# Performance work log

Hardware: AMD Instinct MI355X
Metric: run time of the kernel (lower is better)

The kernel has to match this reference:

```python
import jax, jax.numpy as jnp
import numpy as np

N, E, DIN, H, F = 50000, 800000, 128, 3, 64
NEG_SLOPE = 0.2


def setup_inputs() -> dict:
    key = jax.random.key(0)
    ks = jax.random.split(key, 16)
    p = lambda k, shape: jax.random.normal(k, shape, jnp.float32) * 0.05
    return {
        "feats": jax.random.normal(ks[0], (N, DIN), jnp.float32),
        "src": jax.random.randint(ks[1], (E,), 0, N, jnp.int32),
        "dst": jax.random.randint(ks[2], (E,), 0, N, jnp.int32),
        "W1s": p(ks[3], (DIN, H * F)), "b1s": jnp.zeros((H * F,), jnp.float32),
        "W1d": p(ks[4], (DIN, H * F)), "b1d": jnp.zeros((H * F,), jnp.float32),
        "attn1": p(ks[5], (H, F)), "bias1": jnp.zeros((H * F,), jnp.float32),
        "W2s": p(ks[6], (H * F, H * F)), "b2s": jnp.zeros((H * F,), jnp.float32),
        "W2d": p(ks[7], (H * F, H * F)), "b2d": jnp.zeros((H * F,), jnp.float32),
        "attn2": p(ks[8], (H, F)), "bias2": jnp.zeros((H * F,), jnp.float32),
    }


def gatv2_layer(h, src, dst, Ws, bs, Wd, bd, attn, bias):
    """DGL GATv2Conv: separate src/dst projections, LeakyReLU(el+er) attention,
    edge softmax grouped by destination, scatter-weighted aggregation, bias, tanh."""
    n = h.shape[0]
    fs = (h @ Ws + bs).reshape(n, H, F)   # feat_src [N,H,F]
    fd = (h @ Wd + bd).reshape(n, H, F)   # feat_dst [N,H,F]
    # per-edge attention logits: a . leaky_relu(el[src] + er[dst])  -> [E,H]
    e = jax.nn.leaky_relu(fs[src] + fd[dst], NEG_SLOPE)
    logits = jnp.einsum("ehf,hf->eh", e, attn)
    # numerically-stable edge softmax grouped by dst node
    m = jax.ops.segment_max(logits, dst, num_segments=n)          # [N,H]
    ex = jnp.exp(logits - m[dst])                                  # [E,H]
    denom = jax.ops.segment_sum(ex, dst, num_segments=n)          # [N,H]
    a = ex / denom[dst]                                            # [E,H]
    # weighted scatter-aggregate of source features to destinations
    out = jax.ops.segment_sum(a[:, :, None] * fs[src], dst, num_segments=n)  # [N,H,F]
    out = out + bias.reshape(1, H, F)
    return jnp.tanh(out).reshape(n, H * F)


def reference(feats, src, dst,
              W1s, b1s, W1d, b1d, attn1, bias1,
              W2s, b2s, W2d, b2d, attn2, bias2):
    out0 = feats
    out1 = gatv2_layer(out0, src, dst, W1s, b1s, W1d, b1d, attn1, bias1)
    out2 = gatv2_layer(out1, src, dst, W2s, b2s, W2d, b2d, attn2, bias2)
    return (out0, out1, out2)
```

## Files before the change

### kernel.cpp

```cpp
#include <hip/hip_runtime.h>
#include <hip/hip_bf16.h>

#define NN   50000
#define EE   800000
#define DDIN 128
#define HH   3
#define FF   64
#define HF   192
#define NEG  0.2f
#define LOG2E 1.4426950408889634f

typedef __attribute__((ext_vector_type(8))) short bf16x8;
typedef __attribute__((ext_vector_type(4))) float f32x4;

__device__ __forceinline__ float b2f(ushort u){
  union { uint i; float f; } v; v.i = ((uint)u) << 16; return v.f;
}
__device__ __forceinline__ ushort f2bu(float f){
  __hip_bfloat16 h = __float2bfloat16(f);
  return *reinterpret_cast<ushort*>(&h);
}
__device__ __forceinline__ void us4_to_f(ushort4 u, float* f){
  f[0]=b2f(u.x); f[1]=b2f(u.y); f[2]=b2f(u.z); f[3]=b2f(u.w);
}

#define DPP_ADD(v, ctrl, rmask) \
  v += __int_as_float(__builtin_amdgcn_update_dpp(0, __float_as_int(v), ctrl, rmask, 0xf, true))
#define ROW_SUM(v) do{ \
  DPP_ADD(v, 0x111, 0xf); \
  DPP_ADD(v, 0x112, 0xf); \
  DPP_ADD(v, 0x114, 0xf); \
  DPP_ADD(v, 0x118, 0xf); \
}while(0)
__device__ __forceinline__ float swz_bcast15(float v){
  return __int_as_float(__builtin_amdgcn_ds_swizzle(__float_as_int(v), 0x01F0));
}
__device__ __forceinline__ float xadd16(float v){
  return v + __int_as_float(__builtin_amdgcn_ds_swizzle(__float_as_int(v), 0x401F));
}
__device__ __forceinline__ float xadd32(float v, int bpidx){
  return v + __int_as_float(__builtin_amdgcn_ds_bpermute(bpidx, __float_as_int(v)));
}

__global__ __launch_bounds__(256) void copy_convert_count(
    const float4* __restrict__ in, float4* __restrict__ out,
    ushort4* __restrict__ outb, int n4,
    const int* __restrict__ dst, int* __restrict__ counts){
  int i = blockIdx.x * 256 + threadIdx.x;
  if (i < n4){
    float4 v = in[i];
    out[i] = v;
    ushort4 o;
    o.x = f2bu(v.x); o.y = f2bu(v.y); o.z = f2bu(v.z); o.w = f2bu(v.w);
    outb[i] = o;
  }
  if (i < EE) atomicAdd(&counts[dst[i]], 1);
}

__global__ __launch_bounds__(1024) void scan_local(const int* __restrict__ counts,
                                                   int* __restrict__ row_ptr,
                                                   int* __restrict__ bsums, int n){
  __shared__ int wsum[16];
  int i = blockIdx.x * 1024 + (int)threadIdx.x;
  int lane = threadIdx.x & 63, wid = threadIdx.x >> 6;
  int v = (i < n) ? counts[i] : 0;
  int x = v;
  #pragma unroll
  for (int off = 1; off < 64; off <<= 1){
    int t = __shfl_up(x, off);
    if (lane >= off) x += t;
  }
  if (lane == 63) wsum[wid] = x;
  __syncthreads();
  if (wid == 0 && lane < 16){
    int y = wsum[lane];
    #pragma unroll
    for (int off = 1; off < 16; off <<= 1){
      int t = __shfl_up(y, off);
      if (lane >= off) y += t;
    }
    wsum[lane] = y;
  }
  __syncthreads();
  int incl = x + (wid ? wsum[wid - 1] : 0);
  if (i < n) row_ptr[i + 1] = incl;
  if (threadIdx.x == 1023) bsums[blockIdx.x] = incl;
}

__global__ __launch_bounds__(64) void scan_bsums(int* __restrict__ bsums, int nb){
  int lane = threadIdx.x;
  int v = (lane < nb) ? bsums[lane] : 0;
  int x = v;
  #pragma unroll
  for (int off = 1; off < 64; off <<= 1){
    int t = __shfl_up(x, off);
    if (lane >= off) x += t;
  }
  if (lane < nb) bsums[lane] = x - v;
}

__global__ __launch_bounds__(1024) void scan_add(int* __restrict__ row_ptr,
                                                 const int* __restrict__ bsums, int n){
  int i = blockIdx.x * 1024 + (int)threadIdx.x;
  if (i < n) row_ptr[i + 1] += bsums[blockIdx.x];
  if (i == 0) row_ptr[0] = 0;
}

__global__ __launch_bounds__(256) void scatter_kernel(const int* __restrict__ src,
                                                      const int* __restrict__ dst,
                                                      const int* __restrict__ row_ptr,
                                                      int* __restrict__ cursor,
                                                      int* __restrict__ srcs){
  int e = blockIdx.x * 256 + threadIdx.x;
  if (e >= EE) return;
  int d = dst[e];
  int pos = atomicAdd(&cursor[d], 1);
  srcs[row_ptr[d] + pos] = src[e];
}

__global__ __launch_bounds__(256) void build_wt2(
    const float* __restrict__ W1s, const float* __restrict__ W1d,
    const float* __restrict__ b1s, const float* __restrict__ b1d,
    const float* __restrict__ W2s, const float* __restrict__ W2d,
    const float* __restrict__ b2s, const float* __restrict__ b2d,
    ushort* __restrict__ Wt1, ushort* __restrict__ Wt2,
    float* __restrict__ bcat1, float* __restrict__ bcat2){
  int idx = blockIdx.x * 256 + threadIdx.x;
  if (idx < 384 * DDIN){
    int col = idx / DDIN, k = idx % DDIN;
    float v = (col < HF) ? W1s[(size_t)k * HF + col] : W1d[(size_t)k * HF + col - HF];
    Wt1[idx] = f2bu(v);
  } else if (idx < 384 * (DDIN + HF)){
    int j = idx - 384 * DDIN;
    int col = j / HF, k = j % HF;
    float v = (col < HF) ? W2s[(size_t)k * HF + col] : W2d[(size_t)k * HF + col - HF];
    Wt2[j] = f2bu(v);
  }
  if (idx < 384){
    bcat1[idx] = (idx < HF) ? b1s[idx] : b1d[idx - HF];
    bcat2[idx] = (idx < HF) ? b2s[idx] : b2d[idx - HF];
  }
}

template<int K>
__global__ __launch_bounds__(512, 2) void gemm_persist(
    const ushort* __restrict__ A,
    const ushort* __restrict__ Wt,
    const float* __restrict__ bcat,
    ushort* __restrict__ fsb,
    ushort* __restrict__ fdb,
    int M, int nchunks, int stride){
  constexpr int RB  = K * 2;
  constexpr int CHB = 64 * RB;
  constexpr int NP  = CHB / 8192;
  constexpr int NKK = K / 32;
  __shared__ __align__(16) char lds[2][CHB];
  int tx = threadIdx.x;
  int w = tx >> 6, lane = tx & 63;
  int lr = lane & 15, lq = lane >> 4;

  bf16x8 bfr[3][NKK];
  float4 bv4[3];
  ushort* cb[3];
  #pragma unroll
  for (int ct = 0; ct < 3; ct++){
    int col0 = w * 48 + ct * 16;
    #pragma unroll
    for (int kk = 0; kk < NKK; kk++)
      bfr[ct][kk] = *(const bf16x8*)(Wt + (size_t)(col0 + lr) * K + kk * 32 + lq * 8);
    bv4[ct] = *(const float4*)(bcat + col0 + lq * 4);
    int colbase = col0 + lq * 4;
    cb[ct] = (w < 4) ? (fsb + colbase) : (fdb + colbase - HF);
  }

  int ldsw[NP];
  #pragma unroll
  for (int p = 0; p < NP; p++){
    int s = p * 8192 + tx * 16;
    int r = s / RB, cbyte = s % RB;
    ldsw[p] = r * RB + (cbyte ^ ((r & 7) << 4));
  }

  const char* Ab = (const char*)A;
  int c0 = blockIdx.x;
  if (c0 >= nchunks) return;
  uint4 stg[NP];
  #pragma unroll
  for (int p = 0; p < NP; p++)
    stg[p] = *(const uint4*)(Ab + (size_t)c0 * CHB + p * 8192 + tx * 16);

  int cur = 0;
  for (int c = c0; c < nchunks; c += stride, cur ^= 1){
    char* buf = lds[cur];
    #pragma unroll
    for (int p = 0; p < NP; p++)
      *(uint4*)(buf + ldsw[p]) = stg[p];
    __syncthreads();
    int nc = c + stride;
    if (nc < nchunks){
      #pragma unroll
      for (int p = 0; p < NP; p++)
        stg[p] = *(const uint4*)(Ab + (size_t)nc * CHB + p * 8192 + tx * 16);
    }
    f32x4 acc[4][3];
    #pragma unroll
    for (int rt = 0; rt < 4; rt++)
      #pragma unroll
      for (int ct = 0; ct < 3; ct++)
        acc[rt][ct] = (f32x4){0.f, 0.f, 0.f, 0.f};
    #pragma unroll
    for (int kk = 0; kk < NKK; kk++){
      bf16x8 afr[4];
      #pragma unroll
      for (int rt = 0; rt < 4; rt++){
        int r = rt * 16 + lr;
        int cbyte = kk * 64 + lq * 16;
        afr[rt] = *(const bf16x8*)(buf + r * RB + (cbyte ^ ((r & 7) << 4)));
      }
      #pragma unroll
      for (int rt = 0; rt < 4; rt++)
        #pragma unroll
        for (int ct = 0; ct < 3; ct++)
          acc[rt][ct] = __builtin_amdgcn_mfma_f32_16x16x32_bf16(bfr[ct][kk], afr[rt], acc[rt][ct], 0, 0, 0);
    }
    #pragma unroll
    for (int rt = 0; rt < 4; rt++){
      int row = c * 64 + rt * 16 + lr;
      if (row < M){
        #pragma unroll
        for (int ct = 0; ct < 3; ct++){
          ushort4 o;
          o.x = f2bu(acc[rt][ct][0] + bv4[ct].x);
          o.y = f2bu(acc[rt][ct][1] + bv4[ct].y);
          o.z = f2bu(acc[rt][ct][2] + bv4[ct].z);
          o.w = f2bu(acc[rt][ct][3] + bv4[ct].w);
          *(ushort4*)(cb[ct] + (size_t)row * HF) = o;
        }
      }
    }
  }
}

__global__ __launch_bounds__(256) void node_fused6(
    const ushort* __restrict__ fsb,
    const ushort* __restrict__ fdb,
    const int* __restrict__ row_ptr,
    const int* __restrict__ srcs,
    const float* __restrict__ attn,
    const float* __restrict__ bias,
    float* __restrict__ out,
    ushort* __restrict__ outb){
  int node = (blockIdx.x * 256 + (int)threadIdx.x) >> 6;
  int lane = threadIdx.x & 63;
  if (node >= NN) return;
  int q = lane >> 4;
  int k = lane & 15;
  int r0  = __builtin_amdgcn_readfirstlane(row_ptr[node]);
  int r1  = __builtin_amdgcn_readfirstlane(row_ptr[node + 1]);
  int deg = r1 - r0;
  int bp32 = ((lane ^ 32) << 2);

  const ushort* fdr = fdb + (size_t)node * HF + k * 4;
  float fd[12];
  us4_to_f(*(const ushort4*)(fdr),       fd);
  us4_to_f(*(const ushort4*)(fdr + 64),  fd + 4);
  us4_to_f(*(const ushort4*)(fdr + 128), fd + 8);
  const float* atp = attn + k * 4;
  float4 av0 = *(const float4*)(atp);
  float4 av1 = *(const float4*)(atp + 64);
  float4 av2 = *(const float4*)(atp + 128);
  float at[12] = {av0.x*LOG2E, av0.y*LOG2E, av0.z*LOG2E, av0.w*LOG2E,
                  av1.x*LOG2E, av1.y*LOG2E, av1.z*LOG2E, av1.w*LOG2E,
                  av2.x*LOG2E, av2.y*LOG2E, av2.z*LOG2E, av2.w*LOG2E};

  float s0 = 0.f, s1 = 0.f, s2 = 0.f;
  float acc[12];
  #pragma unroll
  for (int i = 0; i < 12; i++) acc[i] = 0.f;

  if (deg > 0){
    ushort4 cu0, cu1, cu2;
    {
      int ei = r0 + min(q, deg - 1);
      const ushort* p = fsb + (size_t)srcs[ei] * HF + k * 4;
      cu0 = *(const ushort4*)(p);
      cu1 = *(const ushort4*)(p + 64);
      cu2 = *(const ushort4*)(p + 128);
    }
    for (int j = 0; j < deg; j += 4){
      ushort4 nu0 = cu0, nu1 = cu1, nu2 = cu2;
      if (j + 4 < deg){
        int ei = r0 + min(j + 4 + q, deg - 1);
        const ushort* p = fsb + (size_t)srcs[ei] * HF + k * 4;
        nu0 = *(const ushort4*)(p);
        nu1 = *(const ushort4*)(p + 64);
        nu2 = *(const ushort4*)(p + 128);
      }
      float f[12];
      us4_to_f(cu0, f); us4_to_f(cu1, f + 4); us4_to_f(cu2, f + 8);
      float p0 = 0.f, p1 = 0.f, p2 = 0.f;
      #pragma unroll
      for (int i = 0; i < 4; i++){
        float x0 = f[i]     + fd[i];     x0 = fmaxf(x0, NEG * x0); p0 = fmaf(x0, at[i],     p0);
        float x1 = f[4 + i] + fd[4 + i]; x1 = fmaxf(x1, NEG * x1); p1 = fmaf(x1, at[4 + i], p1);
        float x2 = f[8 + i] + fd[8 + i]; x2 = fmaxf(x2, NEG * x2); p2 = fmaf(x2, at[8 + i], p2);
      }
      ROW_SUM(p0); ROW_SUM(p1); ROW_SUM(p2);
      p0 = swz_bcast15(p0); p1 = swz_bcast15(p1); p2 = swz_bcast15(p2);
      bool valid = (j + q) < deg;
      float w0 = valid ? __builtin_amdgcn_exp2f(p0) : 0.f;
      float w1 = valid ? __builtin_amdgcn_exp2f(p1) : 0.f;
      float w2 = valid ? __builtin_amdgcn_exp2f(p2) : 0.f;
      s0 += w0; s1 += w1; s2 += w2;
      #pragma unroll
      for (int i = 0; i < 4; i++){
        acc[i]     = fmaf(w0, f[i],     acc[i]);
        acc[4 + i] = fmaf(w1, f[4 + i], acc[4 + i]);
        acc[8 + i] = fmaf(w2, f[8 + i], acc[8 + i]);
      }
      cu0 = nu0; cu1 = nu1; cu2 = nu2;
    }
  }

  #pragma unroll
  for (int i = 0; i < 12; i++){
    acc[i] = xadd16(acc[i]);
    acc[i] = xadd32(acc[i], bp32);
  }
  s0 = xadd16(s0); s0 = xadd32(s0, bp32);
  s1 = xadd16(s1); s1 = xadd32(s1, bp32);
  s2 = xadd16(s2); s2 = xadd32(s2, bp32);

  float i0 = deg ? 1.f / s0 : 0.f;
  float i1 = deg ? 1.f / s1 : 0.f;
  float i2 = deg ? 1.f / s2 : 0.f;

  if (q == 0){
    const float* bp = bias + k * 4;
    float4 b0 = *(const float4*)(bp);
    float4 b1 = *(const float4*)(bp + 64);
    float4 b2 = *(const float4*)(bp + 128);
    float v[12];
    v[0]  = tanhf(acc[0] * i0 + b0.x);  v[1]  = tanhf(acc[1] * i0 + b0.y);
    v[2]  = tanhf(acc[2] * i0 + b0.z);  v[3]  = tanhf(acc[3] * i0 + b0.w);
    v[4]  = tanhf(acc[4] * i1 + b1.x);  v[5]  = tanhf(acc[5] * i1 + b1.y);
    v[6]  = tanhf(acc[6] * i1 + b1.z);  v[7]  = tanhf(acc[7] * i1 + b1.w);
    v[8]  = tanhf(acc[8] * i2 + b2.x);  v[9]  = tanhf(acc[9] * i2 + b2.y);
    v[10] = tanhf(acc[10] * i2 + b2.z); v[11] = tanhf(acc[11] * i2 + b2.w);
    float* op = out + (size_t)node * HF + k * 4;
    *(float4*)(op)       = make_float4(v[0], v[1], v[2], v[3]);
    *(float4*)(op + 64)  = make_float4(v[4], v[5], v[6], v[7]);
    *(float4*)(op + 128) = make_float4(v[8], v[9], v[10], v[11]);
    if (outb){
      ushort* ob = outb + (size_t)node * HF + k * 4;
      ushort4 o0, o1, o2;
      o0.x = f2bu(v[0]); o0.y = f2bu(v[1]); o0.z = f2bu(v[2]); o0.w = f2bu(v[3]);
      o1.x = f2bu(v[4]); o1.y = f2bu(v[5]); o1.z = f2bu(v[6]); o1.w = f2bu(v[7]);
      o2.x = f2bu(v[8]); o2.y = f2bu(v[9]); o2.z = f2bu(v[10]); o2.w = f2bu(v[11]);
      *(ushort4*)(ob)       = o0;
      *(ushort4*)(ob + 64)  = o1;
      *(ushort4*)(ob + 128) = o2;
    }
  }
}

extern "C" void kernel_launch(void* const* d_in, const int* in_sizes, int n_in,
                              void* d_out, int out_size, void* d_ws, size_t ws_size,
                              hipStream_t stream) {
  const float* feats = (const float*)d_in[0];
  const int*   src   = (const int*)d_in[1];
  const int*   dst   = (const int*)d_in[2];
  const float* W1s = (const float*)d_in[3];  const float* b1s   = (const float*)d_in[4];
  const float* W1d = (const float*)d_in[5];  const float* b1d   = (const float*)d_in[6];
  const float* at1 = (const float*)d_in[7];  const float* bias1 = (const float*)d_in[8];
  const float* W2s = (const float*)d_in[9];  const float* b2s   = (const float*)d_in[10];
  const float* W2d = (const float*)d_in[11]; const float* b2d   = (const float*)d_in[12];
  const float* at2 = (const float*)d_in[13]; const float* bias2 = (const float*)d_in[14];

  float* out  = (float*)d_out;
  float* out1 = out  + (size_t)NN * DDIN;
  float* out2 = out1 + (size_t)NN * HF;

  char* ws = (char*)d_ws;
  ushort* fsb    = (ushort*)ws;                       ws += (size_t)NN * HF * 2;
  ushort* fdb    = (ushort*)ws;                       ws += (size_t)NN * HF * 2;
  ushort* out1b  = (ushort*)ws;                       ws += (size_t)NN * HF * 2;
  ushort* featsb = (ushort*)ws;                       ws += (size_t)NN * DDIN * 2;
  ushort* Wt1    = (ushort*)ws;                       ws += (size_t)384 * DDIN * 2;
  ushort* Wt2    = (ushort*)ws;                       ws += (size_t)384 * HF * 2;
  float*  bcat1  = (float*)ws;                        ws += 384 * 4;
  float*  bcat2  = (float*)ws;                        ws += 384 * 4;
  int*    counts = (int*)ws;                          ws += (size_t)NN * 4;
  int*    row_ptr= (int*)ws;                          ws += (size_t)(NN + 1) * 4;
  int*    srcs   = (int*)ws;                          ws += (size_t)EE * 4;
  int*    bsums  = (int*)ws;

  const int NB = (NN + 1023) / 1024;
  const int NCHUNK = (NN + 63) / 64;
  const int GEMM_GRID = 512;

  const int N4 = NN * DDIN / 4;

  hipMemsetAsync(counts, 0, NN * sizeof(int), stream);
  copy_convert_count<<<(N4 + 255) / 256, 256, 0, stream>>>(
      (const float4*)feats, (float4*)out, (ushort4*)featsb, N4, dst, counts);
  scan_local<<<NB, 1024, 0, stream>>>(counts, row_ptr, bsums, NN);
  scan_bsums<<<1, 64, 0, stream>>>(bsums, NB);
  scan_add<<<NB, 1024, 0, stream>>>(row_ptr, bsums, NN);
  hipMemsetAsync(counts, 0, NN * sizeof(int), stream);
  scatter_kernel<<<(EE + 255) / 256, 256, 0, stream>>>(src, dst, row_ptr, counts, srcs);

  build_wt2<<<(384 * (DDIN + HF) + 255) / 256, 256, 0, stream>>>(
      W1s, W1d, b1s, b1d, W2s, W2d, b2s, b2d, Wt1, Wt2, bcat1, bcat2);

  int node_blocks = (NN + 3) / 4;

  gemm_persist<DDIN><<<GEMM_GRID, 512, 0, stream>>>(featsb, Wt1, bcat1, fsb, fdb, NN, NCHUNK, GEMM_GRID);
  node_fused6<<<node_blocks, 256, 0, stream>>>(fsb, fdb, row_ptr, srcs, at1, bias1, out1, out1b);

  gemm_persist<HF><<<GEMM_GRID, 512, 0, stream>>>(out1b, Wt2, bcat2, fsb, fdb, NN, NCHUNK, GEMM_GRID);
  node_fused6<<<node_blocks, 256, 0, stream>>>(fsb, fdb, row_ptr, srcs, at2, bias2, out2, nullptr);
}
```

Before: 276.6 us.

## Stage GEMM output through LDS for coalesced stores and streamline CSR build

```diff
diff --git a/kernel.cpp b/kernel.cpp
--- a/kernel.cpp
+++ b/kernel.cpp
@@ -45,7 +45,8 @@
 __global__ __launch_bounds__(256) void copy_convert_count(
     const float4* __restrict__ in, float4* __restrict__ out,
     ushort4* __restrict__ outb, int n4,
-    const int* __restrict__ dst, int* __restrict__ counts){
+    const int* __restrict__ dst, int* __restrict__ counts,
+    int* __restrict__ pos){
   int i = blockIdx.x * 256 + threadIdx.x;
   if (i < n4){
     float4 v = in[i];
@@ -54,7 +55,7 @@
     o.x = f2bu(v.x); o.y = f2bu(v.y); o.z = f2bu(v.z); o.w = f2bu(v.w);
     outb[i] = o;
   }
-  if (i < EE) atomicAdd(&counts[dst[i]], 1);
+  if (i < EE) pos[i] = atomicAdd(&counts[dst[i]], 1);
 }
 
 __global__ __launch_bounds__(1024) void scan_local(const int* __restrict__ counts,
@@ -87,8 +88,10 @@
   if (threadIdx.x == 1023) bsums[blockIdx.x] = incl;
 }
 
-__global__ __launch_bounds__(64) void scan_bsums(int* __restrict__ bsums, int nb){
-  int lane = threadIdx.x;
+__global__ __launch_bounds__(1024) void scan_add2(int* __restrict__ row_ptr,
+                                                  const int* __restrict__ bsums,
+                                                  int nb, int n){
+  int lane = threadIdx.x & 63;
   int v = (lane < nb) ? bsums[lane] : 0;
   int x = v;
   #pragma unroll
@@ -96,26 +99,20 @@
     int t = __shfl_up(x, off);
     if (lane >= off) x += t;
   }
-  if (lane < nb) bsums[lane] = x - v;
-}
-
-__global__ __launch_bounds__(1024) void scan_add(int* __restrict__ row_ptr,
-                                                 const int* __restrict__ bsums, int n){
+  int off_b = __shfl(x - v, (int)blockIdx.x);
   int i = blockIdx.x * 1024 + (int)threadIdx.x;
-  if (i < n) row_ptr[i + 1] += bsums[blockIdx.x];
+  if (i < n) row_ptr[i + 1] += off_b;
   if (i == 0) row_ptr[0] = 0;
 }
 
-__global__ __launch_bounds__(256) void scatter_kernel(const int* __restrict__ src,
-                                                      const int* __restrict__ dst,
-                                                      const int* __restrict__ row_ptr,
-                                                      int* __restrict__ cursor,
-                                                      int* __restrict__ srcs){
+__global__ __launch_bounds__(256) void scatter_pos(const int* __restrict__ src,
+                                                   const int* __restrict__ dst,
+                                                   const int* __restrict__ row_ptr,
+                                                   const int* __restrict__ pos,
+                                                   int* __restrict__ srcs){
   int e = blockIdx.x * 256 + threadIdx.x;
   if (e >= EE) return;
-  int d = dst[e];
-  int pos = atomicAdd(&cursor[d], 1);
-  srcs[row_ptr[d] + pos] = src[e];
+  srcs[row_ptr[dst[e]] + pos[e]] = src[e];
 }
 
 __global__ __launch_bounds__(256) void build_wt2(
@@ -154,14 +151,14 @@
   constexpr int CHB = 64 * RB;
   constexpr int NP  = CHB / 8192;
   constexpr int NKK = K / 32;
-  __shared__ __align__(16) char lds[2][CHB];
+  constexpr int CRB = 768;
+  __shared__ __align__(16) char lds[49152];
   int tx = threadIdx.x;
   int w = tx >> 6, lane = tx & 63;
   int lr = lane & 15, lq = lane >> 4;
 
   bf16x8 bfr[3][NKK];
   float4 bv4[3];
-  ushort* cb[3];
   #pragma unroll
   for (int ct = 0; ct < 3; ct++){
     int col0 = w * 48 + ct * 16;
@@ -169,8 +166,6 @@
     for (int kk = 0; kk < NKK; kk++)
       bfr[ct][kk] = *(const bf16x8*)(Wt + (size_t)(col0 + lr) * K + kk * 32 + lq * 8);
     bv4[ct] = *(const float4*)(bcat + col0 + lq * 4);
-    int colbase = col0 + lq * 4;
-    cb[ct] = (w < 4) ? (fsb + colbase) : (fdb + colbase - HF);
   }
 
   int ldsw[NP];
@@ -191,10 +186,10 @@
 
   int cur = 0;
   for (int c = c0; c < nchunks; c += stride, cur ^= 1){
-    char* buf = lds[cur];
+    int boff = cur ? CHB : 0;
     #pragma unroll
     for (int p = 0; p < NP; p++)
-      *(uint4*)(buf + ldsw[p]) = stg[p];
+      *(uint4*)(lds + boff + ldsw[p]) = stg[p];
     __syncthreads();
     int nc = c + stride;
     if (nc < nchunks){
@@ -215,7 +210,7 @@
       for (int rt = 0; rt < 4; rt++){
         int r = rt * 16 + lr;
         int cbyte = kk * 64 + lq * 16;
-        afr[rt] = *(const bf16x8*)(buf + r * RB + (cbyte ^ ((r & 7) << 4)));
+        afr[rt] = *(const bf16x8*)(lds + boff + r * RB + (cbyte ^ ((r & 7) << 4)));
       }
       #pragma unroll
       for (int rt = 0; rt < 4; rt++)
@@ -223,21 +218,36 @@
         for (int ct = 0; ct < 3; ct++)
           acc[rt][ct] = __builtin_amdgcn_mfma_f32_16x16x32_bf16(bfr[ct][kk], afr[rt], acc[rt][ct], 0, 0, 0);
     }
+    __syncthreads();
     #pragma unroll
     for (int rt = 0; rt < 4; rt++){
-      int row = c * 64 + rt * 16 + lr;
+      int r = rt * 16 + lr;
+      int sw = (r & 7) << 4;
+      #pragma unroll
+      for (int ct = 0; ct < 3; ct++){
+        ushort4 o;
+        o.x = f2bu(acc[rt][ct][0] + bv4[ct].x);
+        o.y = f2bu(acc[rt][ct][1] + bv4[ct].y);
+        o.z = f2bu(acc[rt][ct][2] + bv4[ct].z);
+        o.w = f2bu(acc[rt][ct][3] + bv4[ct].w);
+        int cbyte = (w * 48 + ct * 16 + lq * 4) * 2;
+        *(ushort4*)(lds + r * CRB + (cbyte ^ sw)) = o;
+      }
+    }
+    __syncthreads();
+    #pragma unroll
+    for (int p = 0; p < 6; p++){
+      int s = p * 8192 + tx * 16;
+      int r = s / CRB, cbyte = s % CRB;
+      int row = c * 64 + r;
       if (row < M){
-        #pragma unroll
-        for (int ct = 0; ct < 3; ct++){
-          ushort4 o;
-          o.x = f2bu(acc[rt][ct][0] + bv4[ct].x);
-          o.y = f2bu(acc[rt][ct][1] + bv4[ct].y);
-          o.z = f2bu(acc[rt][ct][2] + bv4[ct].z);
-          o.w = f2bu(acc[rt][ct][3] + bv4[ct].w);
-          *(ushort4*)(cb[ct] + (size_t)row * HF) = o;
-        }
-      }
-    }
+        uint4 v = *(const uint4*)(lds + r * CRB + (cbyte ^ ((r & 7) << 4)));
+        char* dstp = (cbyte < 384) ? ((char*)fsb + (size_t)row * 384 + cbyte)
+                                   : ((char*)fdb + (size_t)row * 384 + cbyte - 384);
+        *(uint4*)dstp = v;
+      }
+    }
+    __syncthreads();
   }
 }
 
@@ -393,6 +403,7 @@
   int*    counts = (int*)ws;                          ws += (size_t)NN * 4;
   int*    row_ptr= (int*)ws;                          ws += (size_t)(NN + 1) * 4;
   int*    srcs   = (int*)ws;                          ws += (size_t)EE * 4;
+  int*    pos    = (int*)ws;                          ws += (size_t)EE * 4;
   int*    bsums  = (int*)ws;
 
   const int NB = (NN + 1023) / 1024;
@@ -401,14 +412,12 @@
 
   const int N4 = NN * DDIN / 4;
 
-  hipMemsetAsync(counts, 0, NN * sizeof(int), stream);
+  (void)hipMemsetAsync(counts, 0, NN * sizeof(int), stream);
   copy_convert_count<<<(N4 + 255) / 256, 256, 0, stream>>>(
-      (const float4*)feats, (float4*)out, (ushort4*)featsb, N4, dst, counts);
+      (const float4*)feats, (float4*)out, (ushort4*)featsb, N4, dst, counts, pos);
   scan_local<<<NB, 1024, 0, stream>>>(counts, row_ptr, bsums, NN);
-  scan_bsums<<<1, 64, 0, stream>>>(bsums, NB);
-  scan_add<<<NB, 1024, 0, stream>>>(row_ptr, bsums, NN);
-  hipMemsetAsync(counts, 0, NN * sizeof(int), stream);
-  scatter_kernel<<<(EE + 255) / 256, 256, 0, stream>>>(src, dst, row_ptr, counts, srcs);
+  scan_add2<<<NB, 1024, 0, stream>>>(row_ptr, bsums, NB, NN);
+  scatter_pos<<<(EE + 255) / 256, 256, 0, stream>>>(src, dst, row_ptr, pos, srcs);
 
   build_wt2<<<(384 * (DDIN + HF) + 255) / 256, 256, 0, stream>>>(
       W1s, W1d, b1s, b1d, W2s, W2d, b2s, b2d, Wt1, Wt2, bcat1, bcat2);
```

Result: faster. 248.9 us (-10.0%).
